# Performance work log

Hardware: AMD Instinct MI355X
Metric: run time of the kernel (lower is better)

## Reference

```python
import jax, jax.numpy as jnp
import numpy as np

T, B, V, E, H, L = 70, 64, 10000, 512, 1024, 2


def setup_inputs() -> dict:
    key = jax.random.key(0)
    ks = jax.random.split(key, 10)
    k = float(1.0 / np.sqrt(H))
    u = lambda kk, shape, a: jax.random.uniform(kk, shape, jnp.float32, -a, a)
    return {
        "inputs": jax.random.randint(ks[0], (T, B), 0, V, dtype=jnp.int32),
        "hidden": jnp.zeros((L, B, H), jnp.float32),
        "emb_W": u(ks[1], (V, E), 0.1),
        "Wx0": u(ks[2], (H, E), k),   # nn.Linear weight is [out, in]
        "Wx1": u(ks[3], (H, H), k),
        "Wh0": u(ks[4], (H, H), k),
        "bh0": u(ks[5], (H,), k),
        "Wh1": u(ks[6], (H, H), k),
        "bh1": u(ks[7], (H,), k),
        "Wy": u(ks[8], (V, H), 0.1),
        "by": jnp.zeros((V,), jnp.float32),
    }


def reference(inputs, hidden, emb_W, Wx0, Wx1, Wh0, bh0, Wh1, bh1, Wy, by):
    # Stacked Elman RNN, dropout identity (dp_keep_prob=1.0).
    embedded = emb_W[inputs]  # [T, B, E]

    def step(h, x_t):
        # h: [L, B, H]; x_t: [B, E]
        h0 = jnp.tanh(x_t @ Wx0.T + h[0] @ Wh0.T + bh0)
        h1 = jnp.tanh(h0 @ Wx1.T + h[1] @ Wh1.T + bh1)
        new_h = jnp.stack([h0, h1])  # [L, B, H]
        logits_t = h1 @ Wy.T + by    # [B, V]
        return new_h, logits_t

    h_final, logits = jax.lax.scan(step, hidden, embedded)
    return logits, h_final  # [T, B, V], [L, B, H]
```

## Files before the change

### kernel.cpp

```cpp
#include <hip/hip_runtime.h>
#include <hip/hip_bf16.h>
#include <cmath>
#include <cstdint>


using u16 = unsigned short;
using u32 = unsigned int;
using u64 = unsigned long long;
typedef __attribute__((ext_vector_type(8))) short short8;
typedef __attribute__((ext_vector_type(4))) float f32x4;

#define MFMA_BF16(a, b, c) __builtin_amdgcn_mfma_f32_16x16x32_bf16((a), (b), (c), 0, 0, 0)

__device__ __forceinline__ u16 bf16_rne(float x) {
    u32 u = __float_as_uint(x);
    u32 r = u + 0x7FFFu + ((u >> 16) & 1u);
    return (u16)(r >> 16);
}
__device__ __forceinline__ float bf16_f(u16 h) {
    return __uint_as_float(((u32)h) << 16);
}
__device__ __forceinline__ void split2(float x, u16& hi, u16& lo) {
    hi = bf16_rne(x);
    lo = bf16_rne(x - bf16_f(hi));
}
__device__ __forceinline__ u64 pack4(u16 a, u16 b, u16 c, u16 d) {
    return (u64)a | ((u64)b << 16) | ((u64)c << 32) | ((u64)d << 48);
}

__device__ __forceinline__ void wait_count(int* f, int target) {
    if (threadIdx.x == 0) {
        while (__hip_atomic_load(f, __ATOMIC_RELAXED, __HIP_MEMORY_SCOPE_AGENT) < target)
            __builtin_amdgcn_s_sleep(1);
    }
    __syncthreads();
}
__device__ __forceinline__ void signal_done(int* f) {
    __syncthreads();
    if (threadIdx.x == 0)
        __hip_atomic_fetch_add(f, 1, __ATOMIC_RELAXED, __HIP_MEMORY_SCOPE_AGENT);
}

__global__ __launch_bounds__(256) void split_kernel(
    const float* __restrict__ src, u16* __restrict__ hi, u16* __restrict__ lo, int n4)
{
    int g = blockIdx.x * 256 + threadIdx.x;
    if (g >= n4) return;
    float4 v = *reinterpret_cast<const float4*>(src + (size_t)g * 4);
    u16 h0,h1,h2,h3,l0,l1,l2,l3;
    split2(v.x,h0,l0); split2(v.y,h1,l1); split2(v.z,h2,l2); split2(v.w,h3,l3);
    ushort4 H = {h0,h1,h2,h3}, L = {l0,l1,l2,l3};
    *reinterpret_cast<ushort4*>(hi + (size_t)g * 4) = H;
    *reinterpret_cast<ushort4*>(lo + (size_t)g * 4) = L;
}

__global__ __launch_bounds__(256) void gather_split_kernel(
    const float* __restrict__ emb, const int* __restrict__ idx,
    u16* __restrict__ hi, u16* __restrict__ lo, int n4)
{
    int g = blockIdx.x * 256 + threadIdx.x;
    if (g >= n4) return;
    int m  = g >> 7;
    int c4 = g & 127;
    const float* src = emb + (size_t)idx[m] * 512 + c4 * 4;
    float4 v = *reinterpret_cast<const float4*>(src);
    u16 h0,h1,h2,h3,l0,l1,l2,l3;
    split2(v.x,h0,l0); split2(v.y,h1,l1); split2(v.z,h2,l2); split2(v.w,h3,l3);
    ushort4 H = {h0,h1,h2,h3}, L = {l0,l1,l2,l3};
    size_t o = (size_t)m * 512 + c4 * 4;
    *reinterpret_cast<ushort4*>(hi + o) = H;
    *reinterpret_cast<ushort4*>(lo + o) = L;
}

__global__ __launch_bounds__(256) void gemm_mfma(
    const u16* __restrict__ Ah, const u16* __restrict__ Al,
    const u16* __restrict__ Bh, const u16* __restrict__ Bl,
    const float* __restrict__ bias, float* __restrict__ C,
    int M, int N, int K)
{
    __shared__ u16 sAh[128*32], sAl[128*32], sBh[128*32], sBl[128*32];
    const int tid  = threadIdx.x;
    const int lane = tid & 63;
    const int w    = tid >> 6;
    const int wr   = w >> 1, wc = w & 1;
    const int m0   = blockIdx.y * 128, n0 = blockIdx.x * 128;

    f32x4 acc[4][4];
    #pragma unroll
    for (int i = 0; i < 4; ++i)
        #pragma unroll
        for (int j = 0; j < 4; ++j) acc[i][j] = 0.0f;

    for (int k0 = 0; k0 < K; k0 += 32) {
        #pragma unroll
        for (int r = 0; r < 2; ++r) {
            int s   = r * 256 + tid;
            int row = s >> 2, q = s & 3;
            int gq  = q ^ (row & 3);
            int l16 = row * 32 + q * 8;
            size_t ga = (size_t)(m0 + row) * K + k0 + gq * 8;
            int brow = n0 + row; if (brow >= N) brow = N - 1;
            size_t gb = (size_t)brow * K + k0 + gq * 8;
            *reinterpret_cast<int4*>(sAh + l16) = *reinterpret_cast<const int4*>(Ah + ga);
            *reinterpret_cast<int4*>(sAl + l16) = *reinterpret_cast<const int4*>(Al + ga);
            *reinterpret_cast<int4*>(sBh + l16) = *reinterpret_cast<const int4*>(Bh + gb);
            *reinterpret_cast<int4*>(sBl + l16) = *reinterpret_cast<const int4*>(Bl + gb);
        }
        __syncthreads();

        const int q4 = lane >> 4;
        short8 afh[4], afl[4];
        #pragma unroll
        for (int i = 0; i < 4; ++i) {
            int ra  = wr * 64 + i * 16 + (lane & 15);
            int off = ra * 32 + (q4 ^ (ra & 3)) * 8;
            afh[i] = *reinterpret_cast<const short8*>(sAh + off);
            afl[i] = *reinterpret_cast<const short8*>(sAl + off);
        }
        #pragma unroll
        for (int j = 0; j < 4; ++j) {
            int rb  = wc * 64 + j * 16 + (lane & 15);
            int off = rb * 32 + (q4 ^ (rb & 3)) * 8;
            short8 bfh = *reinterpret_cast<const short8*>(sBh + off);
            short8 bfl = *reinterpret_cast<const short8*>(sBl + off);
            #pragma unroll
            for (int i = 0; i < 4; ++i) {
                acc[i][j] = MFMA_BF16(afh[i], bfh, acc[i][j]);
                acc[i][j] = MFMA_BF16(afh[i], bfl, acc[i][j]);
                acc[i][j] = MFMA_BF16(afl[i], bfh, acc[i][j]);
            }
        }
        __syncthreads();
    }

    #pragma unroll
    for (int j = 0; j < 4; ++j) {
        int n = n0 + wc * 64 + j * 16 + (lane & 15);
        if (n < N) {
            float bv = bias[n];
            #pragma unroll
            for (int i = 0; i < 4; ++i) {
                #pragma unroll
                for (int r = 0; r < 4; ++r) {
                    int m = m0 + wr * 64 + i * 16 + (lane >> 4) * 4 + r;
                    C[(size_t)m * N + n] = acc[i][j][r] + bv;
                }
            }
        }
    }
}

__global__ __launch_bounds__(256, 1) void rnn_persist2(
    const float* __restrict__ A0,
    const u16* __restrict__ hs0h, const u16* __restrict__ hs0l,
    const u16* __restrict__ hs1h, const u16* __restrict__ hs1l,
    u16* __restrict__ H0h, u16* __restrict__ H0l,
    u16* __restrict__ H1h, u16* __restrict__ H1l,
    const u16* __restrict__ Wh0h, const u16* __restrict__ Wh0l,
    const u16* __restrict__ Wx1h, const u16* __restrict__ Wx1l,
    const u16* __restrict__ Wh1h, const u16* __restrict__ Wh1l,
    const float* __restrict__ bh1, int* flags)
{
    __shared__ u16 sW[65536];
    __shared__ float sStage[64 * 17];
    const int tid   = threadIdx.x;
    const int lane  = tid & 63;
    const int w     = tid >> 6;
    const int layer = blockIdx.x >> 6;
    const int n0    = (int)(blockIdx.x & 63) * 16;
    const int m0    = w * 16;
    const int rb    = lane & 15;
    const int q4    = lane >> 4;
    const int arow  = m0 + rb;
    const size_t BH = 65536;
    const int srow  = tid >> 2;
    const int sc4   = (tid & 3) * 4;

    if (layer == 0) {
        for (int i = 0; i < 16; ++i) {
            int s    = i * 256 + tid;
            int arr  = s >> 11;
            int r    = (s >> 7) & 15;
            int g    = s & 127;
            int slot = g ^ (r & 7);
            const u16* src = (arr ? Wh0l : Wh0h) + (size_t)(n0 + r) * 1024 + g * 8;
            *reinterpret_cast<int4*>(sW + arr * 16384 + r * 1024 + slot * 8) =
                *reinterpret_cast<const int4*>(src);
        }
    } else {
        for (int i = 0; i < 32; ++i) {
            int s    = i * 256 + tid;
            int arr  = s >> 12;
            int r    = (s >> 8) & 15;
            int g    = s & 255;
            int slot = g ^ (r & 7);
            const u16* src;
            if (g < 128) src = (arr ? Wx1l : Wx1h) + (size_t)(n0 + r) * 1024 + g * 8;
            else         src = (arr ? Wh1l : Wh1h) + (size_t)(n0 + r) * 1024 + (g - 128) * 8;
            *reinterpret_cast<int4*>(sW + arr * 32768 + r * 2048 + slot * 8) =
                *reinterpret_cast<const int4*>(src);
        }
    }
    __syncthreads();

    if (layer == 0) {
        for (int t = 0; t < 70; ++t) {
            if (t > 0) wait_count(flags + (t - 1), 64);
            const u16* hph = t ? H0h + (size_t)(t - 1) * BH : hs0h;
            const u16* hpl = t ? H0l + (size_t)(t - 1) * BH : hs0l;
            f32x4 acc = {0.f, 0.f, 0.f, 0.f};
            #pragma unroll 8
            for (int kt = 0; kt < 32; ++kt) {
                short8 ah = *reinterpret_cast<const short8*>(hph + (size_t)arow * 1024 + kt * 32 + q4 * 8);
                short8 al = *reinterpret_cast<const short8*>(hpl + (size_t)arow * 1024 + kt * 32 + q4 * 8);
                int slot = (kt * 4 + q4) ^ (rb & 7);
                short8 bh = *reinterpret_cast<const short8*>(sW + rb * 1024 + slot * 8);
                short8 bl = *reinterpret_cast<const short8*>(sW + 16384 + rb * 1024 + slot * 8);
                acc = MFMA_BF16(ah, bh, acc);
                acc = MFMA_BF16(ah, bl, acc);
                acc = MFMA_BF16(al, bh, acc);
            }
            const int n = n0 + rb;
            #pragma unroll
            for (int r = 0; r < 4; ++r) {
                int m = m0 + q4 * 4 + r;
                size_t o = (size_t)t * BH + (size_t)m * 1024 + n;
                sStage[m * 17 + rb] = tanhf(acc[r] + A0[o]);
            }
            __syncthreads();
            {
                float f0 = sStage[srow * 17 + sc4 + 0];
                float f1 = sStage[srow * 17 + sc4 + 1];
                float f2 = sStage[srow * 17 + sc4 + 2];
                float f3 = sStage[srow * 17 + sc4 + 3];
                u16 a,b,c,d, la,lb,lc,ld;
                split2(f0,a,la); split2(f1,b,lb); split2(f2,c,lc); split2(f3,d,ld);
                size_t o64 = ((size_t)t * BH + (size_t)srow * 1024 + n0 + sc4) >> 2;
                __hip_atomic_store((u64*)H0h + o64, pack4(a,b,c,d),
                                   __ATOMIC_RELAXED, __HIP_MEMORY_SCOPE_AGENT);
                __hip_atomic_store((u64*)H0l + o64, pack4(la,lb,lc,ld),
                                   __ATOMIC_RELAXED, __HIP_MEMORY_SCOPE_AGENT);
            }
            signal_done(flags + t);
        }
    } else {
        for (int t = 0; t < 70; ++t) {
            wait_count(flags + t, 64);
            if (t > 0) wait_count(flags + 70 + (t - 1), 64);
            const u16* h0h  = H0h + (size_t)t * BH;
            const u16* h0l  = H0l + (size_t)t * BH;
            const u16* h1ph = t ? H1h + (size_t)(t - 1) * BH : hs1h;
            const u16* h1pl = t ? H1l + (size_t)(t - 1) * BH : hs1l;
            f32x4 acc = {0.f, 0.f, 0.f, 0.f};
            #pragma unroll 8
            for (int kt = 0; kt < 32; ++kt) {
                short8 ah = *reinterpret_cast<const short8*>(h0h + (size_t)arow * 1024 + kt * 32 + q4 * 8);
                short8 al = *reinterpret_cast<const short8*>(h0l + (size_t)arow * 1024 + kt * 32 + q4 * 8);
                int slot = (kt * 4 + q4) ^ (rb & 7);
                short8 bh = *reinterpret_cast<const short8*>(sW + rb * 2048 + slot * 8);
                short8 bl = *reinterpret_cast<const short8*>(sW + 32768 + rb * 2048 + slot * 8);
                acc = MFMA_BF16(ah, bh, acc);
                acc = MFMA_BF16(ah, bl, acc);
                acc = MFMA_BF16(al, bh, acc);
            }
            #pragma unroll 8
            for (int kt = 32; kt < 64; ++kt) {
                int ko = (kt - 32) * 32;
                short8 ah = *reinterpret_cast<const short8*>(h1ph + (size_t)arow * 1024 + ko + q4 * 8);
                short8 al = *reinterpret_cast<const short8*>(h1pl + (size_t)arow * 1024 + ko + q4 * 8);
                int slot = (kt * 4 + q4) ^ (rb & 7);
                short8 bh = *reinterpret_cast<const short8*>(sW + rb * 2048 + slot * 8);
                short8 bl = *reinterpret_cast<const short8*>(sW + 32768 + rb * 2048 + slot * 8);
                acc = MFMA_BF16(ah, bh, acc);
                acc = MFMA_BF16(ah, bl, acc);
                acc = MFMA_BF16(al, bh, acc);
            }
            const int n = n0 + rb;
            #pragma unroll
            for (int r = 0; r < 4; ++r) {
                int m = m0 + q4 * 4 + r;
                sStage[m * 17 + rb] = tanhf(acc[r] + bh1[n]);
            }
            __syncthreads();
            {
                float f0 = sStage[srow * 17 + sc4 + 0];
                float f1 = sStage[srow * 17 + sc4 + 1];
                float f2 = sStage[srow * 17 + sc4 + 2];
                float f3 = sStage[srow * 17 + sc4 + 3];
                u16 a,b,c,d, la,lb,lc,ld;
                split2(f0,a,la); split2(f1,b,lb); split2(f2,c,lc); split2(f3,d,ld);
                size_t o64 = ((size_t)t * BH + (size_t)srow * 1024 + n0 + sc4) >> 2;
                __hip_atomic_store((u64*)H1h + o64, pack4(a,b,c,d),
                                   __ATOMIC_RELAXED, __HIP_MEMORY_SCOPE_AGENT);
                __hip_atomic_store((u64*)H1l + o64, pack4(la,lb,lc,ld),
                                   __ATOMIC_RELAXED, __HIP_MEMORY_SCOPE_AGENT);
            }
            signal_done(flags + 70 + t);
        }
    }
}

__global__ __launch_bounds__(256) void hfinal_kernel(
    const u16* __restrict__ H0h, const u16* __restrict__ H0l,
    const u16* __restrict__ H1h, const u16* __restrict__ H1l,
    float* __restrict__ outp)
{
    int i = blockIdx.x * 256 + threadIdx.x;
    outp[i]         = bf16_f(H0h[i]) + bf16_f(H0l[i]);
    outp[65536 + i] = bf16_f(H1h[i]) + bf16_f(H1l[i]);
}

extern "C" void kernel_launch(void* const* d_in, const int* in_sizes, int n_in,
                              void* d_out, int out_size, void* d_ws, size_t ws_size,
                              hipStream_t stream)
{
    const int*   inputs = (const int*)  d_in[0];
    const float* hidden = (const float*)d_in[1];
    const float* embW   = (const float*)d_in[2];
    const float* Wx0    = (const float*)d_in[3];
    const float* Wx1    = (const float*)d_in[4];
    const float* Wh0    = (const float*)d_in[5];
    const float* bh0    = (const float*)d_in[6];
    const float* Wh1    = (const float*)d_in[7];
    const float* bh1    = (const float*)d_in[8];
    const float* Wy     = (const float*)d_in[9];
    const float* by     = (const float*)d_in[10];
    float* out = (float*)d_out;

    const int T = 70, B = 64, V = 10000, E = 512, H = 1024;
    const int M = T * B;
    const size_t MH = (size_t)M * H;
    const size_t BH = (size_t)B * H;

    char* wsb = (char*)d_ws;
    u16*   Wyh  = (u16*)(wsb);
    u16*   Wyl  = Wyh + (size_t)V * H;
    float* buf0 = (float*)(wsb + 40960000);
    u16*   H0h  = (u16*)(wsb + 59310080);
    u16*   H0l  = H0h + MH;
    u16*   H1h  = H0l + MH;
    u16*   H1l  = H1h + MH;
    u16*   Wx0h = H1l + MH;
    u16*   Wx0l = Wx0h + (size_t)H * E;
    u16*   Wx1h = Wx0l + (size_t)H * E;
    u16*   Wx1l = Wx1h + (size_t)H * H;
    u16*   Wh0h = Wx1l + (size_t)H * H;
    u16*   Wh0l = Wh0h + (size_t)H * H;
    u16*   Wh1h = Wh0l + (size_t)H * H;
    u16*   Wh1l = Wh1h + (size_t)H * H;
    u16*   hs0h = Wh1l + (size_t)H * H;
    u16*   hs0l = hs0h + BH;
    u16*   hs1h = hs0l + BH;
    u16*   hs1l = hs1h + BH;

    u16*   Agh   = (u16*)((char*)d_out + 20971520);
    u16*   Agl   = Agh + (size_t)M * E;
    int*   flags = (int*)((char*)d_out + 104857600);

    dim3 blk(256);

    hipMemsetAsync(flags, 0, 140 * sizeof(int), stream);

    split_kernel<<<dim3((H*E)/1024), blk, 0, stream>>>(Wx0, Wx0h, Wx0l, (H*E)/4);
    split_kernel<<<dim3((H*H)/1024), blk, 0, stream>>>(Wx1, Wx1h, Wx1l, (H*H)/4);
    split_kernel<<<dim3((H*H)/1024), blk, 0, stream>>>(Wh0, Wh0h, Wh0l, (H*H)/4);
    split_kernel<<<dim3((H*H)/1024), blk, 0, stream>>>(Wh1, Wh1h, Wh1l, (H*H)/4);
    split_kernel<<<dim3((V*H)/1024), blk, 0, stream>>>(Wy,  Wyh,  Wyl,  (V*H)/4);
    split_kernel<<<dim3(64), blk, 0, stream>>>(hidden,      hs0h, hs0l, (int)BH/4);
    split_kernel<<<dim3(64), blk, 0, stream>>>(hidden + BH, hs1h, hs1l, (int)BH/4);
    gather_split_kernel<<<dim3((M*E)/1024), blk, 0, stream>>>(embW, inputs, Agh, Agl, (M*E)/4);

    gemm_mfma<<<dim3(H/128, M/128), blk, 0, stream>>>(
        Agh, Agl, Wx0h, Wx0l, bh0, buf0, M, H, E);

    {
        const float* A0p = buf0;
        void* args[] = {
            (void*)&A0p,
            (void*)&hs0h, (void*)&hs0l, (void*)&hs1h, (void*)&hs1l,
            (void*)&H0h,  (void*)&H0l,  (void*)&H1h,  (void*)&H1l,
            (void*)&Wh0h, (void*)&Wh0l, (void*)&Wx1h, (void*)&Wx1l,
            (void*)&Wh1h, (void*)&Wh1l, (void*)&bh1, (void*)&flags
        };
        hipLaunchCooperativeKernel(reinterpret_cast<void*>(rnn_persist2),
                                   dim3(128), blk, args, 0, stream);
    }

    hfinal_kernel<<<dim3(256), blk, 0, stream>>>(
        H0h + (size_t)(T-1) * BH, H0l + (size_t)(T-1) * BH,
        H1h + (size_t)(T-1) * BH, H1l + (size_t)(T-1) * BH,
        out + (size_t)M * V);

    gemm_mfma<<<dim3((V + 127)/128, M/128), blk, 0, stream>>>(
        H1h, H1l, Wyh, Wyl, by, out, M, V, H);
}
```

Before: 1.573 ms.

## Use per-block flag stores and split MFMA accumulators in persistent RNN

Replaces the shared atomic counter per timestep with one flag per producer block. Each block stores its step number, and 64 consumer lanes poll all flags together with a wave-wide vote. This removes serialized atomic adds on one address. It also splits the single MFMA accumulation chain into four independent accumulators, which shortens the dependency chain and lets more loads be in flight. The costs are more polling traffic, since 64 loads go out per check, and higher register pressure from full unrolling.

```diff
diff --git a/kernel.cpp b/kernel.cpp
--- a/kernel.cpp
+++ b/kernel.cpp
@@ -28,17 +28,24 @@
     return (u64)a | ((u64)b << 16) | ((u64)c << 32) | ((u64)d << 48);
 }
 
-__device__ __forceinline__ void wait_count(int* f, int target) {
-    if (threadIdx.x == 0) {
-        while (__hip_atomic_load(f, __ATOMIC_RELAXED, __HIP_MEMORY_SCOPE_AGENT) < target)
+__device__ __forceinline__ void wait_flags(const int* f0, int tgt0,
+                                           const int* f1, int tgt1) {
+    if (threadIdx.x < 64) {
+        for (;;) {
+            int v0 = __hip_atomic_load(f0 + threadIdx.x, __ATOMIC_RELAXED,
+                                       __HIP_MEMORY_SCOPE_AGENT);
+            int v1 = __hip_atomic_load(f1 + threadIdx.x, __ATOMIC_RELAXED,
+                                       __HIP_MEMORY_SCOPE_AGENT);
+            if (__all(v0 >= tgt0) && __all(v1 >= tgt1)) break;
             __builtin_amdgcn_s_sleep(1);
+        }
     }
     __syncthreads();
 }
-__device__ __forceinline__ void signal_done(int* f) {
+__device__ __forceinline__ void signal_flag(int* f, int val) {
     __syncthreads();
     if (threadIdx.x == 0)
-        __hip_atomic_fetch_add(f, 1, __ATOMIC_RELAXED, __HIP_MEMORY_SCOPE_AGENT);
+        __hip_atomic_store(f, val, __ATOMIC_RELAXED, __HIP_MEMORY_SCOPE_AGENT);
 }
 
 __global__ __launch_bounds__(256) void split_kernel(
@@ -150,6 +157,28 @@
     }
 }
 
+#define L0_CHAIN(accv, ktv) { \
+    int kt_ = (ktv); \
+    short8 ah_ = *reinterpret_cast<const short8*>(hph + (size_t)arow * 1024 + kt_ * 32 + q4 * 8); \
+    short8 al_ = *reinterpret_cast<const short8*>(hpl + (size_t)arow * 1024 + kt_ * 32 + q4 * 8); \
+    int slot_ = (kt_ * 4 + q4) ^ (rb & 7); \
+    short8 bh_ = *reinterpret_cast<const short8*>(sW + rb * 1024 + slot_ * 8); \
+    short8 bl_ = *reinterpret_cast<const short8*>(sW + 16384 + rb * 1024 + slot_ * 8); \
+    accv = MFMA_BF16(ah_, bh_, accv); \
+    accv = MFMA_BF16(ah_, bl_, accv); \
+    accv = MFMA_BF16(al_, bh_, accv); }
+
+#define L1_CHAIN(accv, ktv, slotkt, ph, pl) { \
+    int kt_ = (ktv); \
+    short8 ah_ = *reinterpret_cast<const short8*>((ph) + (size_t)arow * 1024 + kt_ * 32 + q4 * 8); \
+    short8 al_ = *reinterpret_cast<const short8*>((pl) + (size_t)arow * 1024 + kt_ * 32 + q4 * 8); \
+    int slot_ = ((slotkt) * 4 + q4) ^ (rb & 7); \
+    short8 bh_ = *reinterpret_cast<const short8*>(sW + rb * 2048 + slot_ * 8); \
+    short8 bl_ = *reinterpret_cast<const short8*>(sW + 32768 + rb * 2048 + slot_ * 8); \
+    accv = MFMA_BF16(ah_, bh_, accv); \
+    accv = MFMA_BF16(ah_, bl_, accv); \
+    accv = MFMA_BF16(al_, bh_, accv); }
+
 __global__ __launch_bounds__(256, 1) void rnn_persist2(
     const float* __restrict__ A0,
     const u16* __restrict__ hs0h, const u16* __restrict__ hs0l,
@@ -167,7 +196,8 @@
     const int lane  = tid & 63;
     const int w     = tid >> 6;
     const int layer = blockIdx.x >> 6;
-    const int n0    = (int)(blockIdx.x & 63) * 16;
+    const int bidx  = (int)(blockIdx.x & 63);
+    const int n0    = bidx * 16;
     const int m0    = w * 16;
     const int rb    = lane & 15;
     const int q4    = lane >> 4;
@@ -175,6 +205,8 @@
     const size_t BH = 65536;
     const int srow  = tid >> 2;
     const int sc4   = (tid & 3) * 4;
+    int* flags0 = flags;
+    int* flags1 = flags + 64;
 
     if (layer == 0) {
         for (int i = 0; i < 16; ++i) {
@@ -205,26 +237,23 @@
 
     if (layer == 0) {
         for (int t = 0; t < 70; ++t) {
-            if (t > 0) wait_count(flags + (t - 1), 64);
+            if (t > 0) wait_flags(flags0, t, flags0, t);
             const u16* hph = t ? H0h + (size_t)(t - 1) * BH : hs0h;
             const u16* hpl = t ? H0l + (size_t)(t - 1) * BH : hs0l;
-            f32x4 acc = {0.f, 0.f, 0.f, 0.f};
-            #pragma unroll 8
-            for (int kt = 0; kt < 32; ++kt) {
-                short8 ah = *reinterpret_cast<const short8*>(hph + (size_t)arow * 1024 + kt * 32 + q4 * 8);
-                short8 al = *reinterpret_cast<const short8*>(hpl + (size_t)arow * 1024 + kt * 32 + q4 * 8);
-                int slot = (kt * 4 + q4) ^ (rb & 7);
-                short8 bh = *reinterpret_cast<const short8*>(sW + rb * 1024 + slot * 8);
-                short8 bl = *reinterpret_cast<const short8*>(sW + 16384 + rb * 1024 + slot * 8);
-                acc = MFMA_BF16(ah, bh, acc);
-                acc = MFMA_BF16(ah, bl, acc);
-                acc = MFMA_BF16(al, bh, acc);
-            }
-            const int n = n0 + rb;
+            f32x4 c0 = {0.f,0.f,0.f,0.f}, c1 = {0.f,0.f,0.f,0.f};
+            f32x4 c2 = {0.f,0.f,0.f,0.f}, c3 = {0.f,0.f,0.f,0.f};
+            #pragma unroll
+            for (int i = 0; i < 8; ++i) {
+                L0_CHAIN(c0, i);
+                L0_CHAIN(c1, 8 + i);
+                L0_CHAIN(c2, 16 + i);
+                L0_CHAIN(c3, 24 + i);
+            }
+            f32x4 acc = (c0 + c1) + (c2 + c3);
             #pragma unroll
             for (int r = 0; r < 4; ++r) {
                 int m = m0 + q4 * 4 + r;
-                size_t o = (size_t)t * BH + (size_t)m * 1024 + n;
+                size_t o = (size_t)t * BH + (size_t)m * 1024 + n0 + rb;
                 sStage[m * 17 + rb] = tanhf(acc[r] + A0[o]);
             }
             __syncthreads();
@@ -241,40 +270,25 @@
                 __hip_atomic_store((u64*)H0l + o64, pack4(la,lb,lc,ld),
                                    __ATOMIC_RELAXED, __HIP_MEMORY_SCOPE_AGENT);
             }
-            signal_done(flags + t);
+            signal_flag(flags0 + bidx, t + 1);
         }
     } else {
         for (int t = 0; t < 70; ++t) {
-            wait_count(flags + t, 64);
-            if (t > 0) wait_count(flags + 70 + (t - 1), 64);
+            wait_flags(flags0, t + 1, flags1, t);
             const u16* h0h  = H0h + (size_t)t * BH;
             const u16* h0l  = H0l + (size_t)t * BH;
             const u16* h1ph = t ? H1h + (size_t)(t - 1) * BH : hs1h;
             const u16* h1pl = t ? H1l + (size_t)(t - 1) * BH : hs1l;
-            f32x4 acc = {0.f, 0.f, 0.f, 0.f};
-            #pragma unroll 8
-            for (int kt = 0; kt < 32; ++kt) {
-                short8 ah = *reinterpret_cast<const short8*>(h0h + (size_t)arow * 1024 + kt * 32 + q4 * 8);
-                short8 al = *reinterpret_cast<const short8*>(h0l + (size_t)arow * 1024 + kt * 32 + q4 * 8);
-                int slot = (kt * 4 + q4) ^ (rb & 7);
-                short8 bh = *reinterpret_cast<const short8*>(sW + rb * 2048 + slot * 8);
-                short8 bl = *reinterpret_cast<const short8*>(sW + 32768 + rb * 2048 + slot * 8);
-                acc = MFMA_BF16(ah, bh, acc);
-                acc = MFMA_BF16(ah, bl, acc);
-                acc = MFMA_BF16(al, bh, acc);
-            }
-            #pragma unroll 8
-            for (int kt = 32; kt < 64; ++kt) {
-                int ko = (kt - 32) * 32;
-                short8 ah = *reinterpret_cast<const short8*>(h1ph + (size_t)arow * 1024 + ko + q4 * 8);
-                short8 al = *reinterpret_cast<const short8*>(h1pl + (size_t)arow * 1024 + ko + q4 * 8);
-                int slot = (kt * 4 + q4) ^ (rb & 7);
-                short8 bh = *reinterpret_cast<const short8*>(sW + rb * 2048 + slot * 8);
-                short8 bl = *reinterpret_cast<const short8*>(sW + 32768 + rb * 2048 + slot * 8);
-                acc = MFMA_BF16(ah, bh, acc);
-                acc = MFMA_BF16(ah, bl, acc);
-                acc = MFMA_BF16(al, bh, acc);
-            }
+            f32x4 c0 = {0.f,0.f,0.f,0.f}, c1 = {0.f,0.f,0.f,0.f};
+            f32x4 c2 = {0.f,0.f,0.f,0.f}, c3 = {0.f,0.f,0.f,0.f};
+            #pragma unroll
+            for (int i = 0; i < 16; ++i) {
+                L1_CHAIN(c0, i,       i,      h0h,  h0l);
+                L1_CHAIN(c1, 16 + i,  16 + i, h0h,  h0l);
+                L1_CHAIN(c2, i,       32 + i, h1ph, h1pl);
+                L1_CHAIN(c3, 16 + i,  48 + i, h1ph, h1pl);
+            }
+            f32x4 acc = (c0 + c1) + (c2 + c3);
             const int n = n0 + rb;
             #pragma unroll
             for (int r = 0; r < 4; ++r) {
@@ -295,7 +309,7 @@
                 __hip_atomic_store((u64*)H1l + o64, pack4(la,lb,lc,ld),
                                    __ATOMIC_RELAXED, __HIP_MEMORY_SCOPE_AGENT);
             }
-            signal_done(flags + 70 + t);
+            signal_flag(flags1 + bidx, t + 1);
         }
     }
 }
@@ -359,7 +373,7 @@
 
     dim3 blk(256);
 
-    hipMemsetAsync(flags, 0, 140 * sizeof(int), stream);
+    hipMemsetAsync(flags, 0, 128 * sizeof(int), stream);
 
     split_kernel<<<dim3((H*E)/1024), blk, 0, stream>>>(Wx0, Wx0h, Wx0l, (H*E)/4);
     split_kernel<<<dim3((H*H)/1024), blk, 0, stream>>>(Wx1, Wx1h, Wx1l, (H*H)/4);
```

Measured after the change: 1.800 ms. 1.14x slower.
